# Performance work log

Hardware: AMD Instinct MI355X
Metric: run time of the kernel (lower is better)

## Reference

```python
import jax, jax.numpy as jnp
import numpy as np

N = 100000
E = 1600000
IN_C, HID_C, OUT_C = 128, 128, 64


def setup_inputs() -> dict:
    key = jax.random.key(0)
    k_x, k_e, k1, k2 = jax.random.split(key, 4)
    x = jax.random.normal(k_x, (N, IN_C), dtype=jnp.float32)
    edge_index = jax.random.randint(k_e, (2, E), 0, N, dtype=jnp.int32)
    # Glorot-style init for GCN weights, zero bias (PyG default)
    W1 = jax.random.normal(k1, (IN_C, HID_C), dtype=jnp.float32) * (1.0 / np.sqrt(IN_C))
    b1 = jnp.zeros((HID_C,), dtype=jnp.float32)
    W2 = jax.random.normal(k2, (HID_C, OUT_C), dtype=jnp.float32) * (1.0 / np.sqrt(HID_C))
    b2 = jnp.zeros((OUT_C,), dtype=jnp.float32)
    return {"x": x, "edge_index": edge_index, "W1": W1, "b1": b1, "W2": W2, "b2": b2}


def _gcn_norm(edge_index, n):
    # PyG gcn_norm: add self-loops, symmetric normalization D^-1/2 A D^-1/2
    loops = jnp.arange(n, dtype=edge_index.dtype)
    row = jnp.concatenate([edge_index[0], loops])  # source nodes
    col = jnp.concatenate([edge_index[1], loops])  # target nodes
    deg = jax.ops.segment_sum(jnp.ones_like(col, dtype=jnp.float32), col, num_segments=n)
    dinv = jnp.where(deg > 0, jax.lax.rsqrt(deg), 0.0)
    norm = dinv[row] * dinv[col]  # [E + N]
    return row, col, norm


def _gcn_conv(h, W, b, row, col, norm, n):
    h = h @ W                              # dense transform first (out_c <= in_c)
    msg = h[row] * norm[:, None]           # gather + scale per edge
    agg = jax.ops.segment_sum(msg, col, num_segments=n)  # scatter-add at targets
    return agg + b


def reference(x, edge_index, W1, b1, W2, b2):
    n = x.shape[0]
    row, col, norm = _gcn_norm(edge_index, n)
    h = jax.nn.relu(_gcn_conv(x, W1, b1, row, col, norm, n))
    mu = _gcn_conv(h, W2, b2, row, col, norm, n)
    return mu
```

## Files before the change

kernel.cpp:

```cpp
#include <hip/hip_runtime.h>
#include <hip/hip_bf16.h>


static inline int cdiv(int a, int b) { return (a + b - 1) / b; }

__device__ inline unsigned short f2bf(float f) {
    __hip_bfloat16 b = __float2bfloat16(f);
    return *(unsigned short*)&b;
}
__device__ inline float2 bf2_to_f2(unsigned int u) {
    return make_float2(__uint_as_float(u << 16),
                       __uint_as_float(u & 0xffff0000u));
}
__device__ inline float bf_to_f(unsigned short u) {
    return __uint_as_float(((unsigned int)u) << 16);
}


__global__ void k_init(int* __restrict__ cnt, int* __restrict__ cursor, int n) {
    int i = blockIdx.x * blockDim.x + threadIdx.x;
    if (i < n) { cnt[i] = 0; cursor[i] = 0; }
}

__global__ void k_deg(const int* __restrict__ col, int* __restrict__ cnt, int e) {
    int i = blockIdx.x * blockDim.x + threadIdx.x;
    if (i < e) atomicAdd(&cnt[col[i]], 1);
}

__global__ void k_dinv(const int* __restrict__ cnt, float* __restrict__ dinv, int n) {
    int i = blockIdx.x * blockDim.x + threadIdx.x;
    if (i < n) dinv[i] = rsqrtf((float)(cnt[i] + 1));
}

__global__ void k_scan1(const int* __restrict__ cnt, int* __restrict__ pref,
                        int* __restrict__ bsum, int n) {
    __shared__ int s[256];
    int t = threadIdx.x;
    int i = blockIdx.x * 256 + t;
    int v = (i < n) ? cnt[i] : 0;
    s[t] = v;
    __syncthreads();
    for (int off = 1; off < 256; off <<= 1) {
        int x = (t >= off) ? s[t - off] : 0;
        __syncthreads();
        s[t] += x;
        __syncthreads();
    }
    if (i < n) pref[i] = s[t] - v;
    if (t == 255) bsum[blockIdx.x] = s[255];
}

__global__ void k_scan2(const int* __restrict__ bsum, int* __restrict__ boff, int nb) {
    __shared__ int s[512];
    int t = threadIdx.x;
    int v = (t < nb) ? bsum[t] : 0;
    s[t] = v;
    __syncthreads();
    for (int off = 1; off < 512; off <<= 1) {
        int x = (t >= off) ? s[t - off] : 0;
        __syncthreads();
        s[t] += x;
        __syncthreads();
    }
    if (t < nb) boff[t] = s[t] - v;
}

__global__ void k_scan3(int* __restrict__ pref, const int* __restrict__ boff,
                        int n, int e_total) {
    int i = blockIdx.x * blockDim.x + threadIdx.x;
    if (i < n) pref[i] += boff[i >> 8];
    if (i == n) pref[n] = e_total;
}

__global__ void k_fill(const int* __restrict__ row, const int* __restrict__ col,
                       const int* __restrict__ indptr, int* __restrict__ cursor,
                       int* __restrict__ csr_row, int e) {
    int i = blockIdx.x * blockDim.x + threadIdx.x;
    if (i >= e) return;
    int c = col[i];
    int pos = indptr[c] + atomicAdd(&cursor[c], 1);
    csr_row[pos] = row[i];
}


template <int COUT>
__global__ __launch_bounds__(256) void gemm_k(const float* __restrict__ X,
                                              const float* __restrict__ W,
                                              const float* __restrict__ dinv,
                                              __hip_bfloat16* __restrict__ G, int n) {
    constexpr int KT = 64;
    constexpr int CG = COUT / 4;
    constexpr int MG = 256 / CG;
    constexpr int TILE_M = MG * 4;
    __shared__ float xs[TILE_M][KT];
    __shared__ float ws[KT][COUT];
    const int t = threadIdx.x;
    const int m_base = blockIdx.x * TILE_M;
    const int tx = t % CG, ty = t / CG;
    const int c0 = tx * 4, m0 = ty * 4;
    float acc[4][4] = {};
    for (int kt = 0; kt < 128; kt += KT) {
        {
            const float4* src = (const float4*)(W + (size_t)kt * COUT);
            float4* dst = (float4*)&ws[0][0];
            constexpr int NW = KT * COUT / 4 / 256;
#pragma unroll
            for (int i = 0; i < NW; i++) dst[t + i * 256] = src[t + i * 256];
        }
        {
            float4* dst = (float4*)&xs[0][0];
            constexpr int NX = TILE_M * KT / 4 / 256;
#pragma unroll
            for (int i = 0; i < NX; i++) {
                int idx = t + i * 256;
                int m = idx >> 4, q = idx & 15;
                int gm = m_base + m;
                float4 v = make_float4(0.f, 0.f, 0.f, 0.f);
                if (gm < n) v = ((const float4*)X)[(size_t)gm * 32 + (kt >> 2) + q];
                dst[idx] = v;
            }
        }
        __syncthreads();
#pragma unroll
        for (int k = 0; k < KT; k += 4) {
            float xr[4][4], wr[4][4];
#pragma unroll
            for (int mm = 0; mm < 4; mm++) {
                float4 v = *(const float4*)&xs[m0 + mm][k];
                xr[mm][0] = v.x; xr[mm][1] = v.y; xr[mm][2] = v.z; xr[mm][3] = v.w;
            }
#pragma unroll
            for (int kk = 0; kk < 4; kk++) {
                float4 v = *(const float4*)&ws[k + kk][c0];
                wr[kk][0] = v.x; wr[kk][1] = v.y; wr[kk][2] = v.z; wr[kk][3] = v.w;
            }
#pragma unroll
            for (int kk = 0; kk < 4; kk++)
#pragma unroll
                for (int mm = 0; mm < 4; mm++)
#pragma unroll
                    for (int cc = 0; cc < 4; cc++)
                        acc[mm][cc] = fmaf(xr[mm][kk], wr[kk][cc], acc[mm][cc]);
        }
        __syncthreads();
    }
#pragma unroll
    for (int mm = 0; mm < 4; mm++) {
        int gm = m_base + m0 + mm;
        if (gm < n) {
            float dv = dinv[gm];
            ushort4 o;
            o.x = f2bf(dv * acc[mm][0]); o.y = f2bf(dv * acc[mm][1]);
            o.z = f2bf(dv * acc[mm][2]); o.w = f2bf(dv * acc[mm][3]);
            *(ushort4*)&G[(size_t)gm * COUT + c0] = o;
        }
    }
}


__global__ __launch_bounds__(256) void k_agg128(const __hip_bfloat16* __restrict__ g,
                                                const int* __restrict__ indptr,
                                                const int* __restrict__ csr_row,
                                                const float* __restrict__ dinv,
                                                const float* __restrict__ bias,
                                                float* __restrict__ out, int n) {
    const int lane = threadIdx.x & 63;
    const int wid0 = (blockIdx.x * blockDim.x + threadIdx.x) >> 6;
    const int nw = (gridDim.x * blockDim.x) >> 6;
    const unsigned int* gp = (const unsigned int*)g;
    const float2 b = ((const float2*)bias)[lane];
    for (int wid = wid0; wid < n; wid += nw) {
        float2 a[8];
#pragma unroll
        for (int k = 0; k < 8; k++) a[k] = make_float2(0.f, 0.f);
        {
            float2 v = bf2_to_f2(gp[(size_t)wid * 64 + lane]);
            a[0] = v;
        }
        int e = indptr[wid], e1 = indptr[wid + 1];
        for (; e + 8 <= e1; e += 8) {
            int r[8];
#pragma unroll
            for (int k = 0; k < 8; k++) r[k] = csr_row[e + k];
#pragma unroll
            for (int k = 0; k < 8; k++) {
                float2 v = bf2_to_f2(gp[(size_t)r[k] * 64 + lane]);
                a[k].x += v.x;
                a[k].y += v.y;
            }
        }
        for (; e < e1; e++) {
            float2 v = bf2_to_f2(gp[(size_t)csr_row[e] * 64 + lane]);
            a[0].x += v.x;
            a[0].y += v.y;
        }
        float dv = dinv[wid];
        float sx = ((a[0].x + a[1].x) + (a[2].x + a[3].x)) +
                   ((a[4].x + a[5].x) + (a[6].x + a[7].x));
        float sy = ((a[0].y + a[1].y) + (a[2].y + a[3].y)) +
                   ((a[4].y + a[5].y) + (a[6].y + a[7].y));
        ((float2*)(out + (size_t)wid * 128))[lane] =
            make_float2(fmaxf(fmaf(dv, sx, b.x), 0.f),
                        fmaxf(fmaf(dv, sy, b.y), 0.f));
    }
}

__global__ __launch_bounds__(256) void k_agg64(const __hip_bfloat16* __restrict__ g,
                                               const int* __restrict__ indptr,
                                               const int* __restrict__ csr_row,
                                               const float* __restrict__ dinv,
                                               const float* __restrict__ bias,
                                               float* __restrict__ out, int n) {
    const int lane = threadIdx.x & 63;
    const int wid0 = (blockIdx.x * blockDim.x + threadIdx.x) >> 6;
    const int nw = (gridDim.x * blockDim.x) >> 6;
    const unsigned short* gp = (const unsigned short*)g;
    const float b = bias[lane];
    for (int wid = wid0; wid < n; wid += nw) {
        float a[8];
#pragma unroll
        for (int k = 0; k < 8; k++) a[k] = 0.f;
        a[0] = bf_to_f(gp[(size_t)wid * 64 + lane]);
        int e = indptr[wid], e1 = indptr[wid + 1];
        for (; e + 8 <= e1; e += 8) {
            int r[8];
#pragma unroll
            for (int k = 0; k < 8; k++) r[k] = csr_row[e + k];
#pragma unroll
            for (int k = 0; k < 8; k++)
                a[k] += bf_to_f(gp[(size_t)r[k] * 64 + lane]);
        }
        for (; e < e1; e++)
            a[0] += bf_to_f(gp[(size_t)csr_row[e] * 64 + lane]);
        float s = ((a[0] + a[1]) + (a[2] + a[3])) + ((a[4] + a[5]) + (a[6] + a[7]));
        out[(size_t)wid * 64 + lane] = fmaf(dinv[wid], s, b);
    }
}


extern "C" void kernel_launch(void* const* d_in, const int* in_sizes, int n_in,
                              void* d_out, int out_size, void* d_ws, size_t ws_size,
                              hipStream_t stream) {
    const float* x  = (const float*)d_in[0];
    const int* ei   = (const int*)d_in[1];
    const float* W1 = (const float*)d_in[2];
    const float* b1 = (const float*)d_in[3];
    const float* W2 = (const float*)d_in[4];
    const float* b2 = (const float*)d_in[5];
    float* out = (float*)d_out;

    const int N = in_sizes[0] / 128;
    const int E = in_sizes[1] / 2;
    const int* row = ei;
    const int* col = ei + E;

    char* p = (char*)d_ws;
    auto carve = [&](size_t bytes) -> void* {
        void* r = (void*)p;
        p += (bytes + 255) & ~(size_t)255;
        return r;
    };
    int*   cnt      = (int*)carve((size_t)N * 4);
    float* dinv     = (float*)carve((size_t)N * 4);
    int*   indptr   = (int*)carve((size_t)(N + 1) * 4);
    int*   bsum     = (int*)carve(512 * 4);
    int*   boff     = (int*)carve(512 * 4);
    int*   cursor   = (int*)carve((size_t)N * 4);
    int*   csr_row  = (int*)carve((size_t)E * 4);
    __hip_bfloat16* g1 = (__hip_bfloat16*)carve((size_t)N * 128 * 2);
    float* h1          = (float*)carve((size_t)N * 128 * 4);
    __hip_bfloat16* g2 = (__hip_bfloat16*)carve((size_t)N * 64 * 2);

    const int NB = cdiv(N, 256);
    const int AGG_BLOCKS = 2048;

    k_init<<<cdiv(N, 256), 256, 0, stream>>>(cnt, cursor, N);
    k_deg<<<cdiv(E, 256), 256, 0, stream>>>(col, cnt, E);
    k_dinv<<<cdiv(N, 256), 256, 0, stream>>>(cnt, dinv, N);
    k_scan1<<<NB, 256, 0, stream>>>(cnt, indptr, bsum, N);
    k_scan2<<<1, 512, 0, stream>>>(bsum, boff, NB);
    k_scan3<<<cdiv(N + 1, 256), 256, 0, stream>>>(indptr, boff, N, E);
    k_fill<<<cdiv(E, 256), 256, 0, stream>>>(row, col, indptr, cursor, csr_row, E);

    gemm_k<128><<<cdiv(N, 32), 256, 0, stream>>>(x, W1, dinv, g1, N);
    k_agg128<<<AGG_BLOCKS, 256, 0, stream>>>(g1, indptr, csr_row, dinv, b1, h1, N);
    gemm_k<64><<<cdiv(N, 64), 256, 0, stream>>>(h1, W2, dinv, g2, N);
    k_agg64<<<AGG_BLOCKS, 256, 0, stream>>>(g2, indptr, csr_row, dinv, b2, out, N);
}
```

Before: 489.3 us.

## Build CSR via two-level bucket sort instead of global atomics and scans

Replaces the per-node degree count, three-kernel scan and global-atomic fill with a coarse bucketing pass (128 nodes per bucket) followed by a per-bucket block that builds a local histogram, scan, indptr, dinv and CSR rows in shared memory. This cuts global atomic contention and kernel launches (seven down to four). In exchange it adds an intermediate pairs buffer with a fixed bucket capacity of 4096, which would overflow if a bucket receives more edges than that, and the k_bscan kernel only handles up to 1024 buckets.

```diff
diff --git a/kernel.cpp b/kernel.cpp
--- a/kernel.cpp
+++ b/kernel.cpp
@@ -3,6 +3,9 @@
 
 
 static inline int cdiv(int a, int b) { return (a + b - 1) / b; }
+
+#define BK_SHIFT 7
+#define BK_CAP   4096
 
 __device__ inline unsigned short f2bf(float f) {
     __hip_bfloat16 b = __float2bfloat16(f);
@@ -17,69 +20,78 @@
 }
 
 
-__global__ void k_init(int* __restrict__ cnt, int* __restrict__ cursor, int n) {
+__global__ void k_initb(int* __restrict__ bcur, int nbuk) {
     int i = blockIdx.x * blockDim.x + threadIdx.x;
-    if (i < n) { cnt[i] = 0; cursor[i] = 0; }
-}
-
-__global__ void k_deg(const int* __restrict__ col, int* __restrict__ cnt, int e) {
-    int i = blockIdx.x * blockDim.x + threadIdx.x;
-    if (i < e) atomicAdd(&cnt[col[i]], 1);
-}
-
-__global__ void k_dinv(const int* __restrict__ cnt, float* __restrict__ dinv, int n) {
-    int i = blockIdx.x * blockDim.x + threadIdx.x;
-    if (i < n) dinv[i] = rsqrtf((float)(cnt[i] + 1));
-}
-
-__global__ void k_scan1(const int* __restrict__ cnt, int* __restrict__ pref,
-                        int* __restrict__ bsum, int n) {
-    __shared__ int s[256];
-    int t = threadIdx.x;
-    int i = blockIdx.x * 256 + t;
-    int v = (i < n) ? cnt[i] : 0;
-    s[t] = v;
-    __syncthreads();
-    for (int off = 1; off < 256; off <<= 1) {
-        int x = (t >= off) ? s[t - off] : 0;
-        __syncthreads();
-        s[t] += x;
-        __syncthreads();
-    }
-    if (i < n) pref[i] = s[t] - v;
-    if (t == 255) bsum[blockIdx.x] = s[255];
-}
-
-__global__ void k_scan2(const int* __restrict__ bsum, int* __restrict__ boff, int nb) {
-    __shared__ int s[512];
-    int t = threadIdx.x;
-    int v = (t < nb) ? bsum[t] : 0;
-    s[t] = v;
-    __syncthreads();
-    for (int off = 1; off < 512; off <<= 1) {
-        int x = (t >= off) ? s[t - off] : 0;
-        __syncthreads();
-        s[t] += x;
-        __syncthreads();
-    }
-    if (t < nb) boff[t] = s[t] - v;
-}
-
-__global__ void k_scan3(int* __restrict__ pref, const int* __restrict__ boff,
-                        int n, int e_total) {
-    int i = blockIdx.x * blockDim.x + threadIdx.x;
-    if (i < n) pref[i] += boff[i >> 8];
-    if (i == n) pref[n] = e_total;
-}
-
-__global__ void k_fill(const int* __restrict__ row, const int* __restrict__ col,
-                       const int* __restrict__ indptr, int* __restrict__ cursor,
-                       int* __restrict__ csr_row, int e) {
+    if (i < nbuk) bcur[i] = 0;
+}
+
+__global__ void k_bucket(const int* __restrict__ row, const int* __restrict__ col,
+                         int* __restrict__ bcur, int2* __restrict__ pairs, int e) {
     int i = blockIdx.x * blockDim.x + threadIdx.x;
     if (i >= e) return;
-    int c = col[i];
-    int pos = indptr[c] + atomicAdd(&cursor[c], 1);
-    csr_row[pos] = row[i];
+    int c = col[i], r = row[i];
+    int b = c >> BK_SHIFT;
+    int p = atomicAdd(&bcur[b], 1);
+    pairs[(size_t)b * BK_CAP + p] = make_int2(r, c);
+}
+
+__global__ void k_bscan(const int* __restrict__ bcnt, int* __restrict__ bbase,
+                        int nbuk) {
+    __shared__ int s[1024];
+    int t = threadIdx.x;
+    int v = (t < nbuk) ? bcnt[t] : 0;
+    s[t] = v;
+    __syncthreads();
+    for (int off = 1; off < 1024; off <<= 1) {
+        int x = (t >= off) ? s[t - off] : 0;
+        __syncthreads();
+        s[t] += x;
+        __syncthreads();
+    }
+    if (t < nbuk) bbase[t] = s[t] - v;
+}
+
+__global__ __launch_bounds__(256) void k_build(const int2* __restrict__ pairs,
+                                               const int* __restrict__ bcnt,
+                                               const int* __restrict__ bbase,
+                                               int* __restrict__ indptr,
+                                               float* __restrict__ dinv,
+                                               int* __restrict__ csr_row,
+                                               int n, int e_total) {
+    __shared__ int hist[128], s[128], lcur[128];
+    const int b = blockIdx.x;
+    const int t = threadIdx.x;
+    const int n0 = b << BK_SHIFT;
+    const int nn = min(128, n - n0);
+    const int ne = bcnt[b];
+    const int base = bbase[b];
+    const int2* pp = pairs + (size_t)b * BK_CAP;
+    if (t < 128) { hist[t] = 0; lcur[t] = 0; }
+    __syncthreads();
+    for (int i = t; i < ne; i += 256)
+        atomicAdd(&hist[pp[i].y & 127], 1);
+    __syncthreads();
+    if (t < 128) s[t] = hist[t];
+    __syncthreads();
+    for (int off = 1; off < 128; off <<= 1) {
+        int x = (t < 128 && t >= off) ? s[t - off] : 0;
+        __syncthreads();
+        if (t < 128) s[t] += x;
+        __syncthreads();
+    }
+    if (t < 128) s[t] -= hist[t];
+    __syncthreads();
+    if (t < nn) {
+        indptr[n0 + t] = base + s[t];
+        dinv[n0 + t] = rsqrtf((float)(hist[t] + 1));
+    }
+    if (b == 0 && t == 0) indptr[n] = e_total;
+    for (int i = t; i < ne; i += 256) {
+        int2 pr = pp[i];
+        int c = pr.y & 127;
+        int p = atomicAdd(&lcur[c], 1);
+        csr_row[base + s[c] + p] = pr.x;
+    }
 }
 
 
@@ -253,6 +265,7 @@
     const int E = in_sizes[1] / 2;
     const int* row = ei;
     const int* col = ei + E;
+    const int NBUK = cdiv(N, 1 << BK_SHIFT);
 
     char* p = (char*)d_ws;
     auto carve = [&](size_t bytes) -> void* {
@@ -260,27 +273,23 @@
         p += (bytes + 255) & ~(size_t)255;
         return r;
     };
-    int*   cnt      = (int*)carve((size_t)N * 4);
+    int*   bcur     = (int*)carve((size_t)NBUK * 4);
+    int*   bbase    = (int*)carve((size_t)NBUK * 4);
+    int*   indptr   = (int*)carve((size_t)(N + 1) * 4);
     float* dinv     = (float*)carve((size_t)N * 4);
-    int*   indptr   = (int*)carve((size_t)(N + 1) * 4);
-    int*   bsum     = (int*)carve(512 * 4);
-    int*   boff     = (int*)carve(512 * 4);
-    int*   cursor   = (int*)carve((size_t)N * 4);
     int*   csr_row  = (int*)carve((size_t)E * 4);
+    int2*  pairs    = (int2*)carve((size_t)NBUK * BK_CAP * 8);
     __hip_bfloat16* g1 = (__hip_bfloat16*)carve((size_t)N * 128 * 2);
     float* h1          = (float*)carve((size_t)N * 128 * 4);
     __hip_bfloat16* g2 = (__hip_bfloat16*)carve((size_t)N * 64 * 2);
 
-    const int NB = cdiv(N, 256);
     const int AGG_BLOCKS = 2048;
 
-    k_init<<<cdiv(N, 256), 256, 0, stream>>>(cnt, cursor, N);
-    k_deg<<<cdiv(E, 256), 256, 0, stream>>>(col, cnt, E);
-    k_dinv<<<cdiv(N, 256), 256, 0, stream>>>(cnt, dinv, N);
-    k_scan1<<<NB, 256, 0, stream>>>(cnt, indptr, bsum, N);
-    k_scan2<<<1, 512, 0, stream>>>(bsum, boff, NB);
-    k_scan3<<<cdiv(N + 1, 256), 256, 0, stream>>>(indptr, boff, N, E);
-    k_fill<<<cdiv(E, 256), 256, 0, stream>>>(row, col, indptr, cursor, csr_row, E);
+    k_initb<<<cdiv(NBUK, 256), 256, 0, stream>>>(bcur, NBUK);
+    k_bucket<<<cdiv(E, 256), 256, 0, stream>>>(row, col, bcur, pairs, E);
+    k_bscan<<<1, 1024, 0, stream>>>(bcur, bbase, NBUK);
+    k_build<<<NBUK, 256, 0, stream>>>(pairs, bcur, bbase, indptr, dinv,
+                                      csr_row, N, E);
 
     gemm_k<128><<<cdiv(N, 32), 256, 0, stream>>>(x, W1, dinv, g1, N);
     k_agg128<<<AGG_BLOCKS, 256, 0, stream>>>(g1, indptr, csr_row, dinv, b1, h1, N);
```

Result: slower. 706.8 us (+44.4%).
